# Optimization experiments

Hardware: AMD Instinct MI355X
Metric: run time of the kernel (lower is better)

Reference implementation:

```python
import jax, jax.numpy as jnp
import numpy as np

D_K = 64
SEQ = 20  # hardcoded by the 20x20 relative-distance matrix in the original module


def _rel_dist_matrix():
    # Md[i, j] = i - j if i < j else -(i - j)  ==  -|i - j|
    idx = jnp.arange(SEQ, dtype=jnp.float32)
    return -jnp.abs(idx[:, None] - idx[None, :])  # [SEQ, SEQ]


def setup_inputs() -> dict:
    key = jax.random.key(0)
    kq, kk, kv, km = jax.random.split(key, 4)
    B, H = 512, 16
    Q = jax.random.normal(kq, (B, H, SEQ, D_K), dtype=jnp.float32)
    K = jax.random.normal(kk, (B, H, SEQ, D_K), dtype=jnp.float32)
    V = jax.random.normal(kv, (B, H, SEQ, D_K), dtype=jnp.float32)
    attn_mask = jax.random.uniform(km, (B, H, SEQ, SEQ), dtype=jnp.float32)
    return {"Q": Q, "K": K, "V": V, "attn_mask": attn_mask}


def reference(Q, K, V, attn_mask):
    scale = 1.0 / np.sqrt(D_K).astype(np.float32)
    # raw exp scores (no max-stabilization, faithful to original)
    scores = jnp.exp(jnp.einsum('bhqd,bhkd->bhqk', Q, K) * scale)
    scores = scores * attn_mask
    attn = scores / (jnp.sum(scores, axis=-1, keepdims=True) + 1e-8)
    context = jnp.einsum('bhqk,bhkd->bhqd', attn, V)
    Md = _rel_dist_matrix()  # [SEQ, SEQ], broadcast over (B, H)
    deAtt = context + jnp.einsum('qk,bhkd->bhqd', Md, V)
    return (deAtt, attn)
```

## Files before the change

kernel.cpp:

```cpp
#include <hip/hip_runtime.h>

#define SEQ 20
#define DK  64
#define NG  16
#define SSTRIDE 24

__global__ __launch_bounds__(256)
void fused_deatt_kernel(const float* __restrict__ Qg,
                        const float* __restrict__ Kg,
                        const float* __restrict__ Vg,
                        const float* __restrict__ Mg,
                        float* __restrict__ deAtt,
                        float* __restrict__ attnOut)
{
    __shared__ float4 sQ[SEQ * NG];
    __shared__ float4 sK[SEQ * NG];
    __shared__ float4 sV[SEQ * NG];
    __shared__ __align__(16) float sS[SEQ * SSTRIDE];
    __shared__ float sRinv[SEQ];

    const int bh  = blockIdx.x;
    const int tid = threadIdx.x;
    const size_t base = (size_t)bh * (SEQ * DK);

    const float4* gq = reinterpret_cast<const float4*>(Qg + base);
    const float4* gk = reinterpret_cast<const float4*>(Kg + base);
    const float4* gv = reinterpret_cast<const float4*>(Vg + base);

    for (int i = tid; i < SEQ * NG; i += 256) {
        const int r = i >> 4;
        const int g = i & 15;
        sQ[(r << 4) | (g ^ (r & 3))]        = gq[i];
        sK[(r << 4) | (g ^ ((r >> 1) & 7))] = gk[i];
        sV[i]                               = gv[i];
    }
    __syncthreads();

    if (tid < 100) {
        const int qt = tid / 10;
        const int kt = tid - qt * 10;
        const int q0 = qt * 2, k0 = kt * 2;
        float a00 = 0.f, a01 = 0.f, a10 = 0.f, a11 = 0.f;
        #pragma unroll
        for (int g = 0; g < NG; ++g) {
            const float4 qa = sQ[(q0 << 4)       | (g ^ (q0 & 3))];
            const float4 qb = sQ[((q0 + 1) << 4) | (g ^ ((q0 + 1) & 3))];
            const float4 ka = sK[(k0 << 4)       | (g ^ (kt & 7))];
            const float4 kb = sK[((k0 + 1) << 4) | (g ^ (kt & 7))];
            a00 += qa.x * ka.x; a00 += qa.y * ka.y; a00 += qa.z * ka.z; a00 += qa.w * ka.w;
            a01 += qa.x * kb.x; a01 += qa.y * kb.y; a01 += qa.z * kb.z; a01 += qa.w * kb.w;
            a10 += qb.x * ka.x; a10 += qb.y * ka.y; a10 += qb.z * ka.z; a10 += qb.w * ka.w;
            a11 += qb.x * kb.x; a11 += qb.y * kb.y; a11 += qb.z * kb.z; a11 += qb.w * kb.w;
        }
        const float scale = 0.125f;
        const float* m = Mg + (size_t)bh * (SEQ * SEQ);
        const float2 m0 = *reinterpret_cast<const float2*>(m + q0 * SEQ + k0);
        const float2 m1 = *reinterpret_cast<const float2*>(m + (q0 + 1) * SEQ + k0);
        sS[q0 * SSTRIDE + k0]           = expf(a00 * scale) * m0.x;
        sS[q0 * SSTRIDE + k0 + 1]       = expf(a01 * scale) * m0.y;
        sS[(q0 + 1) * SSTRIDE + k0]     = expf(a10 * scale) * m1.x;
        sS[(q0 + 1) * SSTRIDE + k0 + 1] = expf(a11 * scale) * m1.y;
    }
    __syncthreads();

    if (tid < SEQ) {
        float s = 0.f;
        #pragma unroll
        for (int k = 0; k < SEQ; ++k) s += sS[tid * SSTRIDE + k];
        sRinv[tid] = 1.0f / (s + 1e-8f);
    }
    __syncthreads();

    if (tid < 100) {
        const int qq = tid / 5;
        const int g4 = (tid - qq * 5) * 4;
        const float4 s = *reinterpret_cast<const float4*>(&sS[qq * SSTRIDE + g4]);
        const float r = sRinv[qq];
        float4 o; o.x = s.x * r; o.y = s.y * r; o.z = s.z * r; o.w = s.w * r;
        *reinterpret_cast<float4*>(attnOut + (size_t)bh * (SEQ * SEQ) + qq * SEQ + g4) = o;
    }

    if (tid < 160) {
        const int qp = tid >> 4;
        const int dg = tid & 15;
        const int q0 = qp * 2, q1 = q0 + 1;
        const float r0 = sRinv[q0], r1 = sRinv[q1];
        float4 acc0 = {0.f, 0.f, 0.f, 0.f};
        float4 acc1 = {0.f, 0.f, 0.f, 0.f};
        #pragma unroll
        for (int k4 = 0; k4 < 5; ++k4) {
            const int kb = k4 * 4;
            const float4 s0 = *reinterpret_cast<const float4*>(&sS[q0 * SSTRIDE + kb]);
            const float4 s1 = *reinterpret_cast<const float4*>(&sS[q1 * SSTRIDE + kb]);
            const float4 v0 = sV[(kb + 0) * NG + dg];
            const float4 v1 = sV[(kb + 1) * NG + dg];
            const float4 v2 = sV[(kb + 2) * NG + dg];
            const float4 v3 = sV[(kb + 3) * NG + dg];
            int d;
            d = q0 - (kb + 0); const float w00 = s0.x * r0 - (float)(d < 0 ? -d : d);
            d = q0 - (kb + 1); const float w01 = s0.y * r0 - (float)(d < 0 ? -d : d);
            d = q0 - (kb + 2); const float w02 = s0.z * r0 - (float)(d < 0 ? -d : d);
            d = q0 - (kb + 3); const float w03 = s0.w * r0 - (float)(d < 0 ? -d : d);
            d = q1 - (kb + 0); const float w10 = s1.x * r1 - (float)(d < 0 ? -d : d);
            d = q1 - (kb + 1); const float w11 = s1.y * r1 - (float)(d < 0 ? -d : d);
            d = q1 - (kb + 2); const float w12 = s1.z * r1 - (float)(d < 0 ? -d : d);
            d = q1 - (kb + 3); const float w13 = s1.w * r1 - (float)(d < 0 ? -d : d);
            acc0.x += w00 * v0.x; acc0.y += w00 * v0.y; acc0.z += w00 * v0.z; acc0.w += w00 * v0.w;
            acc0.x += w01 * v1.x; acc0.y += w01 * v1.y; acc0.z += w01 * v1.z; acc0.w += w01 * v1.w;
            acc0.x += w02 * v2.x; acc0.y += w02 * v2.y; acc0.z += w02 * v2.z; acc0.w += w02 * v2.w;
            acc0.x += w03 * v3.x; acc0.y += w03 * v3.y; acc0.z += w03 * v3.z; acc0.w += w03 * v3.w;
            acc1.x += w10 * v0.x; acc1.y += w10 * v0.y; acc1.z += w10 * v0.z; acc1.w += w10 * v0.w;
            acc1.x += w11 * v1.x; acc1.y += w11 * v1.y; acc1.z += w11 * v1.z; acc1.w += w11 * v1.w;
            acc1.x += w12 * v2.x; acc1.y += w12 * v2.y; acc1.z += w12 * v2.z; acc1.w += w12 * v2.w;
            acc1.x += w13 * v3.x; acc1.y += w13 * v3.y; acc1.z += w13 * v3.z; acc1.w += w13 * v3.w;
        }
        reinterpret_cast<float4*>(deAtt + base + q0 * DK)[dg] = acc0;
        reinterpret_cast<float4*>(deAtt + base + q1 * DK)[dg] = acc1;
    }
}

extern "C" void kernel_launch(void* const* d_in, const int* in_sizes, int n_in,
                              void* d_out, int out_size, void* d_ws, size_t ws_size,
                              hipStream_t stream) {
    const float* Q = (const float*)d_in[0];
    const float* K = (const float*)d_in[1];
    const float* V = (const float*)d_in[2];
    const float* M = (const float*)d_in[3];
    float* out = (float*)d_out;

    const int nbh = in_sizes[0] / (SEQ * DK);
    float* deAtt = out;
    float* attn  = out + (size_t)nbh * SEQ * DK;

    fused_deatt_kernel<<<nbh, 256, 0, stream>>>(Q, K, V, M, deAtt, attn);
}
```

Baseline: 177.8 us.

## Map one wavefront per (b,h) head and read Q/K/V directly from global

Each 256-thread block now processes four (b,h) heads, one per wavefront, replacing one head per block. Block-wide __syncthreads are replaced with wave-level LDS waits. Q, K and V are no longer staged in shared memory; lanes read them straight from global, relying on cache reuse. Lanes are remapped so all 64 compute deAtt with 5 rows each, and expf becomes __expf. The aims are less idle-thread waste, fewer barriers and less LDS traffic, at the cost of redundant global/L1 loads and slightly looser exp accuracy.

```diff
diff --git a/kernel.cpp b/kernel.cpp
--- a/kernel.cpp
+++ b/kernel.cpp
@@ -1,121 +1,135 @@
 #include <hip/hip_runtime.h>
 
-#define SEQ 20
-#define DK  64
-#define NG  16
-#define SSTRIDE 24
+#define SEQ  20
+#define DK   64
+#define SSTR 24
+#define WREG 512
 
-__global__ __launch_bounds__(256)
-void fused_deatt_kernel(const float* __restrict__ Qg,
-                        const float* __restrict__ Kg,
-                        const float* __restrict__ Vg,
-                        const float* __restrict__ Mg,
-                        float* __restrict__ deAtt,
-                        float* __restrict__ attnOut)
+__device__ __forceinline__ void wave_sync_lds() {
+    __builtin_amdgcn_wave_barrier();
+    asm volatile("s_waitcnt lgkmcnt(0)" ::: "memory");
+    __builtin_amdgcn_wave_barrier();
+}
+
+__global__ __launch_bounds__(256, 4)
+void fused_deatt_wave_kernel(const float* __restrict__ Qg,
+                             const float* __restrict__ Kg,
+                             const float* __restrict__ Vg,
+                             const float* __restrict__ Mg,
+                             float* __restrict__ deAtt,
+                             float* __restrict__ attnOut,
+                             int nbh)
 {
-    __shared__ float4 sQ[SEQ * NG];
-    __shared__ float4 sK[SEQ * NG];
-    __shared__ float4 sV[SEQ * NG];
-    __shared__ __align__(16) float sS[SEQ * SSTRIDE];
-    __shared__ float sRinv[SEQ];
+    __shared__ float lds[4 * WREG];
 
-    const int bh  = blockIdx.x;
-    const int tid = threadIdx.x;
+    const int tid  = threadIdx.x;
+    const int wv   = tid >> 6;
+    const int lane = tid & 63;
+    const int bh   = blockIdx.x * 4 + wv;
+    if (bh >= nbh) return;
+
+    float* sS    = lds + wv * WREG;
+    float* sRinv = sS + SEQ * SSTR;
+
     const size_t base = (size_t)bh * (SEQ * DK);
-
     const float4* gq = reinterpret_cast<const float4*>(Qg + base);
     const float4* gk = reinterpret_cast<const float4*>(Kg + base);
     const float4* gv = reinterpret_cast<const float4*>(Vg + base);
+    const float*  m  = Mg + (size_t)bh * (SEQ * SEQ);
 
-    for (int i = tid; i < SEQ * NG; i += 256) {
-        const int r = i >> 4;
-        const int g = i & 15;
-        sQ[(r << 4) | (g ^ (r & 3))]        = gq[i];
-        sK[(r << 4) | (g ^ ((r >> 1) & 7))] = gk[i];
-        sV[i]                               = gv[i];
+    if (lane < 50) {
+        const int qg = lane / 10;
+        const int kg = lane - qg * 10;
+        const int q0 = qg * 4, k0 = kg * 2;
+        float a[4][2] = {};
+        #pragma unroll 4
+        for (int g = 0; g < 16; ++g) {
+            const float4 ka = gk[(k0    ) * 16 + g];
+            const float4 kb = gk[(k0 + 1) * 16 + g];
+            #pragma unroll
+            for (int i = 0; i < 4; ++i) {
+                const float4 qa = gq[(q0 + i) * 16 + g];
+                a[i][0] += qa.x*ka.x + qa.y*ka.y + qa.z*ka.z + qa.w*ka.w;
+                a[i][1] += qa.x*kb.x + qa.y*kb.y + qa.z*kb.z + qa.w*kb.w;
+            }
+        }
+        #pragma unroll
+        for (int i = 0; i < 4; ++i) {
+            const float2 mm = *reinterpret_cast<const float2*>(m + (q0 + i) * SEQ + k0);
+            const float e0 = __expf(a[i][0] * 0.125f) * mm.x;
+            const float e1 = __expf(a[i][1] * 0.125f) * mm.y;
+            *reinterpret_cast<float2*>(sS + (q0 + i) * SSTR + k0) = make_float2(e0, e1);
+        }
     }
-    __syncthreads();
+    wave_sync_lds();
 
-    if (tid < 100) {
-        const int qt = tid / 10;
-        const int kt = tid - qt * 10;
-        const int q0 = qt * 2, k0 = kt * 2;
-        float a00 = 0.f, a01 = 0.f, a10 = 0.f, a11 = 0.f;
+    if (lane < SEQ) {
+        const float4* row = reinterpret_cast<const float4*>(sS + lane * SSTR);
+        const float4 r0 = row[0], r1 = row[1], r2 = row[2], r3 = row[3], r4 = row[4];
+        float s = r0.x + r0.y + r0.z + r0.w
+                + r1.x + r1.y + r1.z + r1.w
+                + r2.x + r2.y + r2.z + r2.w
+                + r3.x + r3.y + r3.z + r3.w
+                + r4.x + r4.y + r4.z + r4.w;
+        sRinv[lane] = 1.0f / (s + 1e-8f);
+    }
+    wave_sync_lds();
+
+    {
+        float4* aout = reinterpret_cast<float4*>(attnOut + (size_t)bh * (SEQ * SEQ));
         #pragma unroll
-        for (int g = 0; g < NG; ++g) {
-            const float4 qa = sQ[(q0 << 4)       | (g ^ (q0 & 3))];
-            const float4 qb = sQ[((q0 + 1) << 4) | (g ^ ((q0 + 1) & 3))];
-            const float4 ka = sK[(k0 << 4)       | (g ^ (kt & 7))];
-            const float4 kb = sK[((k0 + 1) << 4) | (g ^ (kt & 7))];
-            a00 += qa.x * ka.x; a00 += qa.y * ka.y; a00 += qa.z * ka.z; a00 += qa.w * ka.w;
-            a01 += qa.x * kb.x; a01 += qa.y * kb.y; a01 += qa.z * kb.z; a01 += qa.w * kb.w;
-            a10 += qb.x * ka.x; a10 += qb.y * ka.y; a10 += qb.z * ka.z; a10 += qb.w * ka.w;
-            a11 += qb.x * kb.x; a11 += qb.y * kb.y; a11 += qb.z * kb.z; a11 += qb.w * kb.w;
+        for (int r = 0; r < 2; ++r) {
+            const int idx = lane + r * 64;
+            if (idx < 100) {
+                const int q  = idx / 5;
+                const int g4 = idx - q * 5;
+                const float4 s = *reinterpret_cast<const float4*>(sS + q * SSTR + g4 * 4);
+                const float rv = sRinv[q];
+                aout[idx] = make_float4(s.x * rv, s.y * rv, s.z * rv, s.w * rv);
+            }
         }
-        const float scale = 0.125f;
-        const float* m = Mg + (size_t)bh * (SEQ * SEQ);
-        const float2 m0 = *reinterpret_cast<const float2*>(m + q0 * SEQ + k0);
-        const float2 m1 = *reinterpret_cast<const float2*>(m + (q0 + 1) * SEQ + k0);
-        sS[q0 * SSTRIDE + k0]           = expf(a00 * scale) * m0.x;
-        sS[q0 * SSTRIDE + k0 + 1]       = expf(a01 * scale) * m0.y;
-        sS[(q0 + 1) * SSTRIDE + k0]     = expf(a10 * scale) * m1.x;
-        sS[(q0 + 1) * SSTRIDE + k0 + 1] = expf(a11 * scale) * m1.y;
-    }
-    __syncthreads();
-
-    if (tid < SEQ) {
-        float s = 0.f;
-        #pragma unroll
-        for (int k = 0; k < SEQ; ++k) s += sS[tid * SSTRIDE + k];
-        sRinv[tid] = 1.0f / (s + 1e-8f);
-    }
-    __syncthreads();
-
-    if (tid < 100) {
-        const int qq = tid / 5;
-        const int g4 = (tid - qq * 5) * 4;
-        const float4 s = *reinterpret_cast<const float4*>(&sS[qq * SSTRIDE + g4]);
-        const float r = sRinv[qq];
-        float4 o; o.x = s.x * r; o.y = s.y * r; o.z = s.z * r; o.w = s.w * r;
-        *reinterpret_cast<float4*>(attnOut + (size_t)bh * (SEQ * SEQ) + qq * SEQ + g4) = o;
     }
 
-    if (tid < 160) {
-        const int qp = tid >> 4;
-        const int dg = tid & 15;
-        const int q0 = qp * 2, q1 = q0 + 1;
-        const float r0 = sRinv[q0], r1 = sRinv[q1];
-        float4 acc0 = {0.f, 0.f, 0.f, 0.f};
-        float4 acc1 = {0.f, 0.f, 0.f, 0.f};
+    {
+        const int qg = lane >> 4;
+        const int dg = lane & 15;
+        float rv[5];
+        #pragma unroll
+        for (int j = 0; j < 5; ++j) rv[j] = sRinv[qg * 5 + j];
+
+        float4 acc[5];
+        #pragma unroll
+        for (int j = 0; j < 5; ++j) acc[j] = make_float4(0.f, 0.f, 0.f, 0.f);
+
         #pragma unroll
         for (int k4 = 0; k4 < 5; ++k4) {
             const int kb = k4 * 4;
-            const float4 s0 = *reinterpret_cast<const float4*>(&sS[q0 * SSTRIDE + kb]);
-            const float4 s1 = *reinterpret_cast<const float4*>(&sS[q1 * SSTRIDE + kb]);
-            const float4 v0 = sV[(kb + 0) * NG + dg];
-            const float4 v1 = sV[(kb + 1) * NG + dg];
-            const float4 v2 = sV[(kb + 2) * NG + dg];
-            const float4 v3 = sV[(kb + 3) * NG + dg];
-            int d;
-            d = q0 - (kb + 0); const float w00 = s0.x * r0 - (float)(d < 0 ? -d : d);
-            d = q0 - (kb + 1); const float w01 = s0.y * r0 - (float)(d < 0 ? -d : d);
-            d = q0 - (kb + 2); const float w02 = s0.z * r0 - (float)(d < 0 ? -d : d);
-            d = q0 - (kb + 3); const float w03 = s0.w * r0 - (float)(d < 0 ? -d : d);
-            d = q1 - (kb + 0); const float w10 = s1.x * r1 - (float)(d < 0 ? -d : d);
-            d = q1 - (kb + 1); const float w11 = s1.y * r1 - (float)(d < 0 ? -d : d);
-            d = q1 - (kb + 2); const float w12 = s1.z * r1 - (float)(d < 0 ? -d : d);
-            d = q1 - (kb + 3); const float w13 = s1.w * r1 - (float)(d < 0 ? -d : d);
-            acc0.x += w00 * v0.x; acc0.y += w00 * v0.y; acc0.z += w00 * v0.z; acc0.w += w00 * v0.w;
-            acc0.x += w01 * v1.x; acc0.y += w01 * v1.y; acc0.z += w01 * v1.z; acc0.w += w01 * v1.w;
-            acc0.x += w02 * v2.x; acc0.y += w02 * v2.y; acc0.z += w02 * v2.z; acc0.w += w02 * v2.w;
-            acc0.x += w03 * v3.x; acc0.y += w03 * v3.y; acc0.z += w03 * v3.z; acc0.w += w03 * v3.w;
-            acc1.x += w10 * v0.x; acc1.y += w10 * v0.y; acc1.z += w10 * v0.z; acc1.w += w10 * v0.w;
-            acc1.x += w11 * v1.x; acc1.y += w11 * v1.y; acc1.z += w11 * v1.z; acc1.w += w11 * v1.w;
-            acc1.x += w12 * v2.x; acc1.y += w12 * v2.y; acc1.z += w12 * v2.z; acc1.w += w12 * v2.w;
-            acc1.x += w13 * v3.x; acc1.y += w13 * v3.y; acc1.z += w13 * v3.z; acc1.w += w13 * v3.w;
+            const float4 v0 = gv[(kb + 0) * 16 + dg];
+            const float4 v1 = gv[(kb + 1) * 16 + dg];
+            const float4 v2 = gv[(kb + 2) * 16 + dg];
+            const float4 v3 = gv[(kb + 3) * 16 + dg];
+            const float kf0 = (float)(kb + 0), kf1 = (float)(kb + 1);
+            const float kf2 = (float)(kb + 2), kf3 = (float)(kb + 3);
+            #pragma unroll
+            for (int j = 0; j < 5; ++j) {
+                const int q = qg * 5 + j;
+                const float qf = (float)q;
+                const float4 s = *reinterpret_cast<const float4*>(sS + q * SSTR + kb);
+                const float w0 = fmaf(s.x, rv[j], -fabsf(qf - kf0));
+                const float w1 = fmaf(s.y, rv[j], -fabsf(qf - kf1));
+                const float w2 = fmaf(s.z, rv[j], -fabsf(qf - kf2));
+                const float w3 = fmaf(s.w, rv[j], -fabsf(qf - kf3));
+                acc[j].x += w0 * v0.x + w1 * v1.x + w2 * v2.x + w3 * v3.x;
+                acc[j].y += w0 * v0.y + w1 * v1.y + w2 * v2.y + w3 * v3.y;
+                acc[j].z += w0 * v0.z + w1 * v1.z + w2 * v2.z + w3 * v3.z;
+                acc[j].w += w0 * v0.w + w1 * v1.w + w2 * v2.w + w3 * v3.w;
+            }
         }
-        reinterpret_cast<float4*>(deAtt + base + q0 * DK)[dg] = acc0;
-        reinterpret_cast<float4*>(deAtt + base + q1 * DK)[dg] = acc1;
+        #pragma unroll
+        for (int j = 0; j < 5; ++j) {
+            const int q = qg * 5 + j;
+            reinterpret_cast<float4*>(deAtt + base + q * DK)[dg] = acc[j];
+        }
     }
 }
 
@@ -132,5 +146,6 @@
     float* deAtt = out;
     float* attn  = out + (size_t)nbh * SEQ * DK;
 
-    fused_deatt_kernel<<<nbh, 256, 0, stream>>>(Q, K, V, M, deAtt, attn);
+    const int blocks = (nbh + 3) / 4;
+    fused_deatt_wave_kernel<<<blocks, 256, 0, stream>>>(Q, K, V, M, deAtt, attn, nbh);
 }
```

New measurement: 278.2 us. 56.5% more time.
